# Performance work log

Measured on AMD Instinct MI355X. Metric: run time of the kernel, lower is better.

## Reference

```python
import jax, jax.numpy as jnp
import numpy as np

B, N, DIM = 4, 2048, 128
HEADS, HEAD = 8, 128
INNER = HEADS * HEAD  # 1024
EPS = 1e-5


def setup_inputs() -> dict:
    key = jax.random.key(0)
    k0, k1, k2 = jax.random.split(key, 3)
    return {
        "x": jax.random.normal(k0, (B, N, DIM), jnp.float32),
        "ln_gamma": jnp.ones((DIM,), jnp.float32),
        "ln_beta": jnp.zeros((DIM,), jnp.float32),
        "w_qkv": jax.random.normal(k1, (3 * INNER, DIM), jnp.float32) * (DIM ** -0.5),
        "w_out": jax.random.normal(k2, (DIM, INNER), jnp.float32) * (INNER ** -0.5),
        "b_out": jnp.zeros((DIM,), jnp.float32),
    }


def _rope(t):
    """lucidrains-style rotary embedding over full last dim of t: [b,h,n,d]."""
    n, d = t.shape[-2], t.shape[-1]
    inv_freq = 1.0 / (10000.0 ** (jnp.arange(0, d, 2, dtype=jnp.float32) / d))
    freqs = jnp.arange(n, dtype=jnp.float32)[:, None] * inv_freq[None, :]  # [n, d/2]
    freqs = jnp.repeat(freqs, 2, axis=-1)  # interleaved duplicate -> [n, d]
    cos, sin = jnp.cos(freqs), jnp.sin(freqs)
    # rotate_half on interleaved pairs: (x1, x2) -> (-x2, x1)
    x1, x2 = t[..., 0::2], t[..., 1::2]
    rot = jnp.stack((-x2, x1), axis=-1).reshape(t.shape)
    return t * cos + rot * sin


def reference(x, ln_gamma, ln_beta, w_qkv, w_out, b_out):
    # LayerNorm
    mu = x.mean(-1, keepdims=True)
    var = x.var(-1, keepdims=True)
    xn = (x - mu) * jax.lax.rsqrt(var + EPS) * ln_gamma + ln_beta
    # QKV projection (bias-free)
    qkv = jnp.einsum('bnd,ed->bne', xn, w_qkv)  # [B, N, 3*INNER]
    q, k, v = jnp.split(qkv, 3, axis=-1)
    to_heads = lambda t: t.reshape(B, N, HEADS, HEAD).transpose(0, 2, 1, 3)
    q, k, v = to_heads(q), to_heads(k), to_heads(v)  # [B, H, N, HEAD]
    # Partial RoPE: rotate all but the last token; last token stays unrotated
    q = jnp.concatenate([_rope(q[:, :, :-1]), q[:, :, -1:]], axis=2)
    k = jnp.concatenate([_rope(k[:, :, :-1]), k[:, :, -1:]], axis=2)
    scale = HEAD ** -0.5
    dots = jnp.einsum('bhid,bhjd->bhij', q, k) * scale  # [B, H, N, N]
    attn = jax.nn.softmax(dots, axis=-1)
    out = jnp.einsum('bhij,bhjd->bhid', attn, v)
    out = out.transpose(0, 2, 1, 3).reshape(B, N, INNER)
    return out @ w_out.T + b_out
```

## Files before the change

kernel.cpp:

```cpp
#include <hip/hip_runtime.h>
#include <hip/hip_bf16.h>
#include <hip/hip_fp16.h>

#define B_      4
#define N_      2048
#define DIM_    128
#define HEADS_  8
#define HEAD_   128
#define INNER_  1024
#define QKV_    3072
#define EPS_    1e-5f
#define SCALE_  0.08838834764831845f
#define ROPE_C  0.20762050593046015f

typedef __attribute__((ext_vector_type(8))) short short8;
typedef __attribute__((ext_vector_type(4))) short short4v;
typedef __attribute__((ext_vector_type(4))) float f32x4;


__device__ __forceinline__ unsigned short f2bf(float f) {
    unsigned u = __builtin_bit_cast(unsigned, f);
    u = (u + 0x7fffu + ((u >> 16) & 1u)) >> 16;
    return (unsigned short)u;
}
__device__ __forceinline__ float bf2f(unsigned short h) {
    unsigned u = ((unsigned)h) << 16;
    return __builtin_bit_cast(float, u);
}
__device__ __forceinline__ unsigned pk2(float a, float b) {
    return (unsigned)f2bf(a) | ((unsigned)f2bf(b) << 16);
}
__device__ __forceinline__ short4v pack4(const float* e) {
    __hip_bfloat162 h0 = __float22bfloat162_rn(make_float2(e[0], e[1]));
    __hip_bfloat162 h1 = __float22bfloat162_rn(make_float2(e[2], e[3]));
    uint2 u;
    __builtin_memcpy(&u.x, &h0, 4);
    __builtin_memcpy(&u.y, &h1, 4);
    return __builtin_bit_cast(short4v, u);
}

__global__ __launch_bounds__(256) void k_ln(
    const float* __restrict__ x, const float* __restrict__ g,
    const float* __restrict__ be, unsigned short* __restrict__ xnb)
{
    const int w = threadIdx.x >> 6, l = threadIdx.x & 63;
    const int row = blockIdx.x * 4 + w;
    float2 v = *(const float2*)(x + (size_t)row * 128 + l * 2);
    float s = v.x + v.y, s2 = v.x * v.x + v.y * v.y;
#pragma unroll
    for (int off = 1; off < 64; off <<= 1) {
        s  += __shfl_xor(s, off);
        s2 += __shfl_xor(s2, off);
    }
    float mu = s * (1.f / 128.f);
    float var = s2 * (1.f / 128.f) - mu * mu;
    float rs = rsqrtf(var + EPS_);
    float2 gg = *(const float2*)(g + l * 2);
    float2 bb = *(const float2*)(be + l * 2);
    float ox = (v.x - mu) * rs * gg.x + bb.x;
    float oy = (v.y - mu) * rs * gg.y + bb.y;
    *(unsigned*)(xnb + (size_t)row * 128 + l * 2) = pk2(ox, oy);
}

__global__ __launch_bounds__(256) void k_cvt(
    const float* __restrict__ src, unsigned short* __restrict__ dst)
{
    size_t i = ((size_t)blockIdx.x * 256 + threadIdx.x) * 8;
    float4 f0 = *(const float4*)(src + i), f1 = *(const float4*)(src + i + 4);
    uint4 u = { pk2(f0.x, f0.y), pk2(f0.z, f0.w), pk2(f1.x, f1.y), pk2(f1.z, f1.w) };
    *(uint4*)(dst + i) = u;
}

__global__ __launch_bounds__(256) void k_qkvf(
    const unsigned short* __restrict__ xnb, const unsigned short* __restrict__ wb,
    unsigned short* __restrict__ Q, unsigned short* __restrict__ K,
    unsigned short* __restrict__ Vt)
{
    __shared__ unsigned short lA[128 * 136];
    __shared__ unsigned short lB[128 * 136];
    const int t = threadIdx.x;
    const int wv = t >> 6, l = t & 63;
    const int lm = l & 15, quad = l >> 4;
    const int row0 = blockIdx.x * 128;
    const int by   = blockIdx.y;
    const int e0   = by * 128;

#pragma unroll
    for (int i = 0; i < 8; ++i) {
        int c = t + 256 * i;  int r = c >> 4, c8 = c & 15;
        *(uint4*)&lA[r * 136 + c8 * 8] =
            *(const uint4*)(xnb + (size_t)(row0 + r) * 128 + c8 * 8);
        *(uint4*)&lB[r * 136 + c8 * 8] =
            *(const uint4*)(wb + (size_t)(e0 + r) * 128 + c8 * 8);
    }
    __syncthreads();

    short8 af[2][4];
#pragma unroll
    for (int mt = 0; mt < 2; ++mt)
#pragma unroll
        for (int ks = 0; ks < 4; ++ks)
            af[mt][ks] = *(short8*)&lA[(wv * 32 + mt * 16 + lm) * 136 + ks * 32 + quad * 8];

    f32x4 acc[2][8];
#pragma unroll
    for (int mt = 0; mt < 2; ++mt)
#pragma unroll
        for (int ct = 0; ct < 8; ++ct) acc[mt][ct] = (f32x4){0.f, 0.f, 0.f, 0.f};
#pragma unroll
    for (int ks = 0; ks < 4; ++ks) {
#pragma unroll
        for (int ct = 0; ct < 8; ++ct) {
            short8 b = *(short8*)&lB[(ct * 16 + lm) * 136 + ks * 32 + quad * 8];
            acc[0][ct] = __builtin_amdgcn_mfma_f32_16x16x32_bf16(af[0][ks], b, acc[0][ct], 0, 0, 0);
            acc[1][ct] = __builtin_amdgcn_mfma_f32_16x16x32_bf16(af[1][ks], b, acc[1][ct], 0, 0, 0);
        }
    }
    __syncthreads();

    const int b  = row0 >> 11;
    const int n0 = row0 & (N_ - 1);
    const int h  = by & 7;
    const int bh = b * 8 + h;

    if (by < 16) {
#pragma unroll
        for (int mt = 0; mt < 2; ++mt)
#pragma unroll
            for (int ct = 0; ct < 8; ++ct)
#pragma unroll
                for (int r = 0; r < 4; ++r)
                    lA[(wv * 32 + mt * 16 + quad * 4 + r) * 136 + ct * 16 + lm] =
                        f2bf(acc[mt][ct][r]);
        __syncthreads();

        const int r_loc = t >> 1, half = t & 1;
        const int n = n0 + r_loc;
        unsigned short* dst = (by < 8 ? Q : K) +
            ((size_t)bh * N_ + n) * HEAD_ + half * 64;
        const bool dorope = (n != N_ - 1);
#pragma unroll
        for (int j = 0; j < 8; ++j) {
            short8 vv = *(short8*)&lA[r_loc * 136 + half * 64 + j * 8];
            if (dorope) {
                unsigned short* pv = (unsigned short*)&vv;
#pragma unroll
                for (int p = 0; p < 4; ++p) {
                    int i0 = half * 32 + j * 4 + p;
                    float invf = exp2f(-(float)i0 * ROPE_C);
                    float th = (float)n * invf;
                    float cs = __cosf(th), sn = __sinf(th);
                    float e = bf2f(pv[2 * p]), o = bf2f(pv[2 * p + 1]);
                    pv[2 * p]     = f2bf(e * cs - o * sn);
                    pv[2 * p + 1] = f2bf(o * cs + e * sn);
                }
            }
            *(short8*)(dst + j * 8) = vv;
        }
    } else {
#pragma unroll
        for (int mt = 0; mt < 2; ++mt)
#pragma unroll
            for (int ct = 0; ct < 8; ++ct)
#pragma unroll
                for (int r = 0; r < 4; ++r)
                    lA[(ct * 16 + lm) * 136 + wv * 32 + quad * 8 + mt * 4 + r] =
                        f2bf(acc[mt][ct][r]);
        __syncthreads();

        const int d = t >> 1, half = t & 1;
        unsigned short* dst = Vt + ((size_t)bh * HEAD_ + d) * N_ + n0 + half * 64;
#pragma unroll
        for (int j = 0; j < 8; ++j)
            *(short8*)(dst + j * 8) = *(short8*)&lA[d * 136 + half * 64 + j * 8];
    }
}

__global__ __launch_bounds__(256) void k_attn(
    const unsigned short* __restrict__ Q, const unsigned short* __restrict__ K,
    const unsigned short* __restrict__ Vt, unsigned short* __restrict__ Ob)
{
    __shared__ unsigned short lK[64 * 136];
    __shared__ unsigned short lV[128 * 68];

    const int t = threadIdx.x;
    const int w = t >> 6, l = t & 63;
    const int lm = l & 15, quad = l >> 4;
    const int bid = blockIdx.x;
    const int bh = bid & 31;
    const int qt = bid >> 5;
    const int n0 = qt * 128;
    const unsigned short* Qb = Q  + (size_t)bh * N_ * HEAD_;
    const unsigned short* Kb = K  + (size_t)bh * N_ * HEAD_;
    const unsigned short* Vb = Vt + (size_t)bh * N_ * HEAD_;

    short8 aq[2][4];
#pragma unroll
    for (int tt = 0; tt < 2; ++tt) {
        const unsigned short* qp =
            Qb + ((size_t)(n0 + tt * 64 + w * 16 + lm)) * 128 + quad * 8;
#pragma unroll
        for (int ks = 0; ks < 4; ++ks)
            aq[tt][ks] = *(const short8*)(qp + ks * 32);
    }

    f32x4 Oa[2][8];
#pragma unroll
    for (int tt = 0; tt < 2; ++tt)
#pragma unroll
        for (int i = 0; i < 8; ++i) Oa[tt][i] = (f32x4){0.f, 0.f, 0.f, 0.f};
    float ps0 = 0.f, ps1 = 0.f;
    const float C1 = SCALE_ * 1.44269504f;
    const float C0 = -23.08312f;

    short8 kr[4], vr[4];
#pragma unroll
    for (int i = 0; i < 4; ++i) {
        int c = t + 256 * i;
        kr[i] = *(const short8*)(Kb + ((size_t)(c >> 4)) * 128 + (c & 15) * 8);
        vr[i] = *(const short8*)(Vb + (size_t)(c >> 3) * N_ + (c & 7) * 8);
    }

    for (int jt = 0; jt < 32; ++jt) {
        __syncthreads();
#pragma unroll
        for (int i = 0; i < 4; ++i) {
            int c = t + 256 * i;
            *(short8*)&lK[(c >> 4) * 136 + (c & 15) * 8] = kr[i];
            *(short8*)&lV[(c >> 3) * 68  + (c & 7)  * 8] = vr[i];
        }
        __syncthreads();
        if (jt < 31) {
#pragma unroll
            for (int i = 0; i < 4; ++i) {
                int c = t + 256 * i;
                kr[i] = *(const short8*)(Kb + ((size_t)((jt + 1) * 64 + (c >> 4))) * 128 + (c & 15) * 8);
                vr[i] = *(const short8*)(Vb + (size_t)(c >> 3) * N_ + (jt + 1) * 64 + (c & 7) * 8);
            }
        }

        short4v pf0[4], pf1[4];
#pragma unroll
        for (int nb = 0; nb < 4; ++nb) {
            f32x4 st0 = (f32x4){0.f, 0.f, 0.f, 0.f};
            f32x4 st1 = (f32x4){0.f, 0.f, 0.f, 0.f};
#pragma unroll
            for (int ks = 0; ks < 4; ++ks) {
                short8 kf = *(short8*)&lK[(nb * 16 + lm) * 136 + ks * 32 + quad * 8];
                st0 = __builtin_amdgcn_mfma_f32_16x16x32_bf16(kf, aq[0][ks], st0, 0, 0, 0);
                st1 = __builtin_amdgcn_mfma_f32_16x16x32_bf16(kf, aq[1][ks], st1, 0, 0, 0);
            }
            float e0[4], e1[4];
#pragma unroll
            for (int r = 0; r < 4; ++r) {
                e0[r] = exp2f(st0[r] * C1 + C0);
                e1[r] = exp2f(st1[r] * C1 + C0);
                ps0 += e0[r];  ps1 += e1[r];
            }
            pf0[nb] = pack4(e0);
            pf1[nb] = pack4(e1);
        }

#pragma unroll
        for (int c2 = 0; c2 < 2; ++c2) {
            short8 ap0 = __builtin_shufflevector(pf0[2 * c2], pf0[2 * c2 + 1],
                                                 0, 1, 2, 3, 4, 5, 6, 7);
            short8 ap1 = __builtin_shufflevector(pf1[2 * c2], pf1[2 * c2 + 1],
                                                 0, 1, 2, 3, 4, 5, 6, 7);
#pragma unroll
            for (int nb8 = 0; nb8 < 8; ++nb8) {
                short8 bv = *(short8*)&lV[(nb8 * 16 + lm) * 68 + c2 * 32 + quad * 8];
                Oa[0][nb8] = __builtin_amdgcn_mfma_f32_16x16x32_bf16(ap0, bv, Oa[0][nb8], 0, 0, 0);
                Oa[1][nb8] = __builtin_amdgcn_mfma_f32_16x16x32_bf16(ap1, bv, Oa[1][nb8], 0, 0, 0);
            }
        }
    }

    ps0 += __shfl_xor(ps0, 16);  ps0 += __shfl_xor(ps0, 32);
    ps1 += __shfl_xor(ps1, 16);  ps1 += __shfl_xor(ps1, 32);

    const int b = bh >> 3, h = bh & 7;
#pragma unroll
    for (int tt = 0; tt < 2; ++tt)
#pragma unroll
        for (int r = 0; r < 4; ++r) {
            float lsum = __shfl(tt == 0 ? ps0 : ps1, (l & 48) | (quad * 4 + r));
            float il = 1.f / lsum;
            int n = n0 + tt * 64 + w * 16 + quad * 4 + r;
            unsigned short* op = Ob + ((size_t)b * N_ + n) * INNER_ + h * HEAD_ + lm;
#pragma unroll
            for (int nb8 = 0; nb8 < 8; ++nb8)
                op[nb8 * 16] = f2bf(Oa[tt][nb8][r] * il);
        }
}

__global__ __launch_bounds__(256) void k_proj(
    const unsigned short* __restrict__ Ob, const unsigned short* __restrict__ wob,
    const float* __restrict__ bias, float* __restrict__ out)
{
    __shared__ unsigned short lA[64 * 136];
    __shared__ unsigned short lB[64 * 136];
    float* lCf = (float*)lA;
    const int t = threadIdx.x;
    const int wv = t >> 6, l = t & 63;
    const int lm = l & 15, quad = l >> 4;
    const int row0 = blockIdx.x * 64;
    const int e0   = blockIdx.y * 64;

    f32x4 acc[4];
#pragma unroll
    for (int ct = 0; ct < 4; ++ct) acc[ct] = (f32x4){0.f, 0.f, 0.f, 0.f};

    for (int kt = 0; kt < 8; ++kt) {
        __syncthreads();
#pragma unroll
        for (int i = 0; i < 4; ++i) {
            int c = t + 256 * i;  int r = c >> 4, c8 = c & 15;
            *(uint4*)&lA[r * 136 + c8 * 8] =
                *(const uint4*)(Ob + (size_t)(row0 + r) * 1024 + kt * 128 + c8 * 8);
            *(uint4*)&lB[r * 136 + c8 * 8] =
                *(const uint4*)(wob + (size_t)(e0 + r) * 1024 + kt * 128 + c8 * 8);
        }
        __syncthreads();
        short8 a_[4];
#pragma unroll
        for (int ks = 0; ks < 4; ++ks)
            a_[ks] = *(short8*)&lA[(wv * 16 + lm) * 136 + ks * 32 + quad * 8];
#pragma unroll
        for (int ks = 0; ks < 4; ++ks)
#pragma unroll
            for (int ct = 0; ct < 4; ++ct) {
                short8 b = *(short8*)&lB[(ct * 16 + lm) * 136 + ks * 32 + quad * 8];
                acc[ct] = __builtin_amdgcn_mfma_f32_16x16x32_bf16(a_[ks], b, acc[ct], 0, 0, 0);
            }
    }
    __syncthreads();
#pragma unroll
    for (int ct = 0; ct < 4; ++ct)
#pragma unroll
        for (int r = 0; r < 4; ++r)
            lCf[(wv * 16 + quad * 4 + r) * 68 + ct * 16 + lm] = acc[ct][r];
    __syncthreads();
#pragma unroll
    for (int i = 0; i < 4; ++i) {
        int c = t + 256 * i;  int r = c >> 4, c4 = c & 15;
        float4 v = *(float4*)&lCf[r * 68 + c4 * 4];
        float4 b4 = *(const float4*)(bias + e0 + c4 * 4);
        v.x += b4.x; v.y += b4.y; v.z += b4.z; v.w += b4.w;
        *(float4*)(out + (size_t)(row0 + r) * 128 + e0 + c4 * 4) = v;
    }
}

extern "C" void kernel_launch(void* const* d_in, const int* in_sizes, int n_in,
                              void* d_out, int out_size, void* d_ws, size_t ws_size,
                              hipStream_t stream) {
    const float* x      = (const float*)d_in[0];
    const float* gamma  = (const float*)d_in[1];
    const float* beta   = (const float*)d_in[2];
    const float* w_qkv  = (const float*)d_in[3];
    const float* w_out  = (const float*)d_in[4];
    const float* b_out  = (const float*)d_in[5];
    float* out = (float*)d_out;
    char* wsb = (char*)d_ws;
    unsigned short* Q    = (unsigned short*)(wsb);
    unsigned short* K    = (unsigned short*)(wsb + (16ull << 20));
    unsigned short* Vt   = (unsigned short*)(wsb + (32ull << 20));
    unsigned short* Ob   = (unsigned short*)(wsb + (48ull << 20));
    unsigned short* xnb  = (unsigned short*)(wsb + (96ull << 20));
    unsigned short* wqb  = (unsigned short*)(wsb + (98ull << 20));
    unsigned short* wob  = (unsigned short*)(wsb + (99ull << 20));

    k_ln       <<<dim3(2048),    256, 0, stream>>>(x, gamma, beta, xnb);
    k_cvt      <<<dim3(192),     256, 0, stream>>>(w_qkv, wqb);
    k_cvt      <<<dim3(64),      256, 0, stream>>>(w_out, wob);
    k_qkvf     <<<dim3(64, 24),  256, 0, stream>>>(xnb, wqb, Q, K, Vt);
    k_attn     <<<dim3(512),     256, 0, stream>>>(Q, K, Vt, Ob);
    k_proj     <<<dim3(128, 2),  256, 0, stream>>>(Ob, wob, b_out, out);
}
```

Baseline: 193.7 us.

## Fuse prep kernels, XOR-swizzle QKV LDS, halve projection tile rows

Merges the LayerNorm and two weight-conversion kernels into one launch, which removes two kernel launches and their gaps. The QKV GEMM's LDS tiles drop the padded stride and use an XOR chunk swizzle instead, cutting LDS footprint and aiming to avoid bank conflicts. The output projection moves to 32-row tiles with four waves splitting columns, doubling the grid to improve occupancy. These are small kernels next to attention, so the overall effect is likely small.

```diff
diff --git a/kernel.cpp b/kernel.cpp
--- a/kernel.cpp
+++ b/kernel.cpp
@@ -39,36 +39,42 @@
     return __builtin_bit_cast(short4v, u);
 }
 
-__global__ __launch_bounds__(256) void k_ln(
+__global__ __launch_bounds__(256) void k_prep(
     const float* __restrict__ x, const float* __restrict__ g,
-    const float* __restrict__ be, unsigned short* __restrict__ xnb)
+    const float* __restrict__ be, const float* __restrict__ w_qkv,
+    const float* __restrict__ w_out, unsigned short* __restrict__ xnb,
+    unsigned short* __restrict__ wqb, unsigned short* __restrict__ wob)
 {
-    const int w = threadIdx.x >> 6, l = threadIdx.x & 63;
-    const int row = blockIdx.x * 4 + w;
-    float2 v = *(const float2*)(x + (size_t)row * 128 + l * 2);
-    float s = v.x + v.y, s2 = v.x * v.x + v.y * v.y;
-#pragma unroll
-    for (int off = 1; off < 64; off <<= 1) {
-        s  += __shfl_xor(s, off);
-        s2 += __shfl_xor(s2, off);
-    }
-    float mu = s * (1.f / 128.f);
-    float var = s2 * (1.f / 128.f) - mu * mu;
-    float rs = rsqrtf(var + EPS_);
-    float2 gg = *(const float2*)(g + l * 2);
-    float2 bb = *(const float2*)(be + l * 2);
-    float ox = (v.x - mu) * rs * gg.x + bb.x;
-    float oy = (v.y - mu) * rs * gg.y + bb.y;
-    *(unsigned*)(xnb + (size_t)row * 128 + l * 2) = pk2(ox, oy);
-}
-
-__global__ __launch_bounds__(256) void k_cvt(
-    const float* __restrict__ src, unsigned short* __restrict__ dst)
-{
-    size_t i = ((size_t)blockIdx.x * 256 + threadIdx.x) * 8;
-    float4 f0 = *(const float4*)(src + i), f1 = *(const float4*)(src + i + 4);
-    uint4 u = { pk2(f0.x, f0.y), pk2(f0.z, f0.w), pk2(f1.x, f1.y), pk2(f1.z, f1.w) };
-    *(uint4*)(dst + i) = u;
+    const int bid = blockIdx.x;
+    if (bid < 2048) {
+        const int w = threadIdx.x >> 6, l = threadIdx.x & 63;
+        const int row = bid * 4 + w;
+        float2 v = *(const float2*)(x + (size_t)row * 128 + l * 2);
+        float s = v.x + v.y, s2 = v.x * v.x + v.y * v.y;
+#pragma unroll
+        for (int off = 1; off < 64; off <<= 1) {
+            s  += __shfl_xor(s, off);
+            s2 += __shfl_xor(s2, off);
+        }
+        float mu = s * (1.f / 128.f);
+        float var = s2 * (1.f / 128.f) - mu * mu;
+        float rs = rsqrtf(var + EPS_);
+        float2 gg = *(const float2*)(g + l * 2);
+        float2 bb = *(const float2*)(be + l * 2);
+        float ox = (v.x - mu) * rs * gg.x + bb.x;
+        float oy = (v.y - mu) * rs * gg.y + bb.y;
+        *(unsigned*)(xnb + (size_t)row * 128 + l * 2) = pk2(ox, oy);
+    } else if (bid < 2240) {
+        size_t i = ((size_t)(bid - 2048) * 256 + threadIdx.x) * 8;
+        float4 f0 = *(const float4*)(w_qkv + i), f1 = *(const float4*)(w_qkv + i + 4);
+        uint4 u = { pk2(f0.x, f0.y), pk2(f0.z, f0.w), pk2(f1.x, f1.y), pk2(f1.z, f1.w) };
+        *(uint4*)(wqb + i) = u;
+    } else {
+        size_t i = ((size_t)(bid - 2240) * 256 + threadIdx.x) * 8;
+        float4 f0 = *(const float4*)(w_out + i), f1 = *(const float4*)(w_out + i + 4);
+        uint4 u = { pk2(f0.x, f0.y), pk2(f0.z, f0.w), pk2(f1.x, f1.y), pk2(f1.z, f1.w) };
+        *(uint4*)(wob + i) = u;
+    }
 }
 
 __global__ __launch_bounds__(256) void k_qkvf(
@@ -76,8 +82,8 @@
     unsigned short* __restrict__ Q, unsigned short* __restrict__ K,
     unsigned short* __restrict__ Vt)
 {
-    __shared__ unsigned short lA[128 * 136];
-    __shared__ unsigned short lB[128 * 136];
+    __shared__ unsigned short lA[128 * 128];
+    __shared__ unsigned short lB[128 * 128];
     const int t = threadIdx.x;
     const int wv = t >> 6, l = t & 63;
     const int lm = l & 15, quad = l >> 4;
@@ -88,9 +94,10 @@
 #pragma unroll
     for (int i = 0; i < 8; ++i) {
         int c = t + 256 * i;  int r = c >> 4, c8 = c & 15;
-        *(uint4*)&lA[r * 136 + c8 * 8] =
+        int sc = (c8 ^ (r & 7)) * 8;
+        *(uint4*)&lA[r * 128 + sc] =
             *(const uint4*)(xnb + (size_t)(row0 + r) * 128 + c8 * 8);
-        *(uint4*)&lB[r * 136 + c8 * 8] =
+        *(uint4*)&lB[r * 128 + sc] =
             *(const uint4*)(wb + (size_t)(e0 + r) * 128 + c8 * 8);
     }
     __syncthreads();
@@ -99,8 +106,10 @@
 #pragma unroll
     for (int mt = 0; mt < 2; ++mt)
 #pragma unroll
-        for (int ks = 0; ks < 4; ++ks)
-            af[mt][ks] = *(short8*)&lA[(wv * 32 + mt * 16 + lm) * 136 + ks * 32 + quad * 8];
+        for (int ks = 0; ks < 4; ++ks) {
+            int r = wv * 32 + mt * 16 + lm;
+            af[mt][ks] = *(short8*)&lA[r * 128 + (((ks * 4 + quad) ^ (r & 7)) << 3)];
+        }
 
     f32x4 acc[2][8];
 #pragma unroll
@@ -111,7 +120,8 @@
     for (int ks = 0; ks < 4; ++ks) {
 #pragma unroll
         for (int ct = 0; ct < 8; ++ct) {
-            short8 b = *(short8*)&lB[(ct * 16 + lm) * 136 + ks * 32 + quad * 8];
+            int r = ct * 16 + lm;
+            short8 b = *(short8*)&lB[r * 128 + (((ks * 4 + quad) ^ (r & 7)) << 3)];
             acc[0][ct] = __builtin_amdgcn_mfma_f32_16x16x32_bf16(af[0][ks], b, acc[0][ct], 0, 0, 0);
             acc[1][ct] = __builtin_amdgcn_mfma_f32_16x16x32_bf16(af[1][ks], b, acc[1][ct], 0, 0, 0);
         }
@@ -129,9 +139,12 @@
 #pragma unroll
             for (int ct = 0; ct < 8; ++ct)
 #pragma unroll
-                for (int r = 0; r < 4; ++r)
-                    lA[(wv * 32 + mt * 16 + quad * 4 + r) * 136 + ct * 16 + lm] =
+                for (int r = 0; r < 4; ++r) {
+                    int row = wv * 32 + mt * 16 + quad * 4 + r;
+                    int chunk = ct * 2 + (lm >> 3);
+                    lA[row * 128 + ((chunk ^ (row & 7)) << 3) + (lm & 7)] =
                         f2bf(acc[mt][ct][r]);
+                }
         __syncthreads();
 
         const int r_loc = t >> 1, half = t & 1;
@@ -141,7 +154,7 @@
         const bool dorope = (n != N_ - 1);
 #pragma unroll
         for (int j = 0; j < 8; ++j) {
-            short8 vv = *(short8*)&lA[r_loc * 136 + half * 64 + j * 8];
+            short8 vv = *(short8*)&lA[r_loc * 128 + (((half * 8 + j) ^ (r_loc & 7)) << 3)];
             if (dorope) {
                 unsigned short* pv = (unsigned short*)&vv;
 #pragma unroll
@@ -163,16 +176,20 @@
 #pragma unroll
             for (int ct = 0; ct < 8; ++ct)
 #pragma unroll
-                for (int r = 0; r < 4; ++r)
-                    lA[(ct * 16 + lm) * 136 + wv * 32 + quad * 8 + mt * 4 + r] =
+                for (int r = 0; r < 4; ++r) {
+                    int row = ct * 16 + lm;
+                    int chunk = wv * 4 + quad;
+                    lA[row * 128 + ((chunk ^ (row & 7)) << 3) + mt * 4 + r] =
                         f2bf(acc[mt][ct][r]);
+                }
         __syncthreads();
 
         const int d = t >> 1, half = t & 1;
         unsigned short* dst = Vt + ((size_t)bh * HEAD_ + d) * N_ + n0 + half * 64;
 #pragma unroll
         for (int j = 0; j < 8; ++j)
-            *(short8*)(dst + j * 8) = *(short8*)&lA[d * 136 + half * 64 + j * 8];
+            *(short8*)(dst + j * 8) =
+                *(short8*)&lA[d * 128 + (((half * 8 + j) ^ (d & 7)) << 3)];
     }
 }
 
@@ -298,26 +315,31 @@
     const unsigned short* __restrict__ Ob, const unsigned short* __restrict__ wob,
     const float* __restrict__ bias, float* __restrict__ out)
 {
-    __shared__ unsigned short lA[64 * 136];
+    __shared__ unsigned short lA[32 * 136];
     __shared__ unsigned short lB[64 * 136];
     float* lCf = (float*)lA;
     const int t = threadIdx.x;
     const int wv = t >> 6, l = t & 63;
     const int lm = l & 15, quad = l >> 4;
-    const int row0 = blockIdx.x * 64;
+    const int rt = wv & 1, ch = wv >> 1;
+    const int row0 = blockIdx.x * 32;
     const int e0   = blockIdx.y * 64;
 
-    f32x4 acc[4];
-#pragma unroll
-    for (int ct = 0; ct < 4; ++ct) acc[ct] = (f32x4){0.f, 0.f, 0.f, 0.f};
+    f32x4 acc[2];
+#pragma unroll
+    for (int ct = 0; ct < 2; ++ct) acc[ct] = (f32x4){0.f, 0.f, 0.f, 0.f};
 
     for (int kt = 0; kt < 8; ++kt) {
         __syncthreads();
 #pragma unroll
-        for (int i = 0; i < 4; ++i) {
+        for (int i = 0; i < 2; ++i) {
             int c = t + 256 * i;  int r = c >> 4, c8 = c & 15;
             *(uint4*)&lA[r * 136 + c8 * 8] =
                 *(const uint4*)(Ob + (size_t)(row0 + r) * 1024 + kt * 128 + c8 * 8);
+        }
+#pragma unroll
+        for (int i = 0; i < 4; ++i) {
+            int c = t + 256 * i;  int r = c >> 4, c8 = c & 15;
             *(uint4*)&lB[r * 136 + c8 * 8] =
                 *(const uint4*)(wob + (size_t)(e0 + r) * 1024 + kt * 128 + c8 * 8);
         }
@@ -325,24 +347,24 @@
         short8 a_[4];
 #pragma unroll
         for (int ks = 0; ks < 4; ++ks)
-            a_[ks] = *(short8*)&lA[(wv * 16 + lm) * 136 + ks * 32 + quad * 8];
+            a_[ks] = *(short8*)&lA[(rt * 16 + lm) * 136 + ks * 32 + quad * 8];
 #pragma unroll
         for (int ks = 0; ks < 4; ++ks)
 #pragma unroll
-            for (int ct = 0; ct < 4; ++ct) {
-                short8 b = *(short8*)&lB[(ct * 16 + lm) * 136 + ks * 32 + quad * 8];
+            for (int ct = 0; ct < 2; ++ct) {
+                short8 b = *(short8*)&lB[(ch * 32 + ct * 16 + lm) * 136 + ks * 32 + quad * 8];
                 acc[ct] = __builtin_amdgcn_mfma_f32_16x16x32_bf16(a_[ks], b, acc[ct], 0, 0, 0);
             }
     }
     __syncthreads();
 #pragma unroll
-    for (int ct = 0; ct < 4; ++ct)
+    for (int ct = 0; ct < 2; ++ct)
 #pragma unroll
         for (int r = 0; r < 4; ++r)
-            lCf[(wv * 16 + quad * 4 + r) * 68 + ct * 16 + lm] = acc[ct][r];
+            lCf[(rt * 16 + quad * 4 + r) * 68 + ch * 32 + ct * 16 + lm] = acc[ct][r];
     __syncthreads();
 #pragma unroll
-    for (int i = 0; i < 4; ++i) {
+    for (int i = 0; i < 2; ++i) {
         int c = t + 256 * i;  int r = c >> 4, c4 = c & 15;
         float4 v = *(float4*)&lCf[r * 68 + c4 * 4];
         float4 b4 = *(const float4*)(bias + e0 + c4 * 4);
@@ -370,10 +392,9 @@
     unsigned short* wqb  = (unsigned short*)(wsb + (98ull << 20));
     unsigned short* wob  = (unsigned short*)(wsb + (99ull << 20));
 
-    k_ln       <<<dim3(2048),    256, 0, stream>>>(x, gamma, beta, xnb);
-    k_cvt      <<<dim3(192),     256, 0, stream>>>(w_qkv, wqb);
-    k_cvt      <<<dim3(64),      256, 0, stream>>>(w_out, wob);
-    k_qkvf     <<<dim3(64, 24),  256, 0, stream>>>(xnb, wqb, Q, K, Vt);
-    k_attn     <<<dim3(512),     256, 0, stream>>>(Q, K, Vt, Ob);
-    k_proj     <<<dim3(128, 2),  256, 0, stream>>>(Ob, wob, b_out, out);
-}
+    k_prep <<<dim3(2304),    256, 0, stream>>>(x, gamma, beta, w_qkv, w_out,
+                                               xnb, wqb, wob);
+    k_qkvf <<<dim3(64, 24),  256, 0, stream>>>(xnb, wqb, Q, K, Vt);
+    k_attn <<<dim3(512),     256, 0, stream>>>(Q, K, Vt, Ob);
+    k_proj <<<dim3(256, 2),  256, 0, stream>>>(Ob, wob, b_out, out);
+}
```

Measured after the change: 188.7 us (median of 3 runs). -2.6%, faster.
